# Kernel tuning notes

Measured on AMD Instinct MI355X. Metric: run time of the kernel, lower is better.

Reference implementation:

```python
import jax, jax.numpy as jnp
import numpy as np

N = 100000      # nodes
E = 1600000     # edges (avg degree 16)
FEAT, HID, OUT = 128, 64, 40
P_DROP = 0.5


def setup_inputs() -> dict:
    key = jax.random.key(0)
    ks = jax.random.split(key, 7)
    x = jax.random.normal(ks[0], (N, FEAT), dtype=jnp.float32)
    edge_index = jax.random.randint(ks[1], (2, E), 0, N, dtype=jnp.int32)
    W1 = jax.random.normal(ks[2], (FEAT, HID), dtype=jnp.float32) / np.float32(np.sqrt(FEAT))
    b1 = jnp.zeros((HID,), jnp.float32)
    W2 = jax.random.normal(ks[3], (HID, OUT), dtype=jnp.float32) / np.float32(np.sqrt(HID))
    b2 = jnp.zeros((OUT,), jnp.float32)
    # scaled inverted-dropout mask: values in {0, 1/(1-p)}
    keep = jax.random.bernoulli(ks[4], 1.0 - P_DROP, (N, HID))
    drop_mask = keep.astype(jnp.float32) / np.float32(1.0 - P_DROP)
    return {"x": x, "edge_index": edge_index, "W1": W1, "b1": b1,
            "W2": W2, "b2": b2, "drop_mask": drop_mask}


def _gcn_conv(x, W, b, src, dst):
    """PyG GCNConv: h = xW; add self-loops; sym-normalized scatter-add; +b."""
    h = x @ W                                   # [N, D_out]
    ones = jnp.ones((src.shape[0],), h.dtype)
    deg = jax.ops.segment_sum(ones, dst, num_segments=N) + 1.0  # +1 self-loop
    dinv = jax.lax.rsqrt(deg)                   # deg > 0 due to self-loops
    norm = dinv[src] * dinv[dst]                # [E]
    msg = h[src] * norm[:, None]                # gather + scale
    agg = jax.ops.segment_sum(msg, dst, num_segments=N)
    agg = agg + h * (dinv * dinv)[:, None]      # self-loop contribution
    return agg + b


def reference(x, edge_index, W1, b1, W2, b2, drop_mask):
    src, dst = edge_index[0], edge_index[1]
    h = _gcn_conv(x, W1, b1, src, dst)
    h = jax.nn.relu(h)
    h = h * drop_mask                           # F.dropout (pre-drawn mask)
    out = _gcn_conv(h, W2, b2, src, dst)
    return out
```

## Files before the change

kernel.cpp:

```cpp
#include <hip/hip_runtime.h>
#include <hip/hip_fp16.h>

#define NN     100000
#define NE     1600000
#define FEAT   128
#define HID    64
#define OUTD   40
#define BSH    8
#define BNODES 256
#define NBKT   ((NN + BNODES - 1) / BNODES)
#define CAP    5120
#define CCHUNK 2048

typedef _Float16 half8 __attribute__((ext_vector_type(8)));
typedef float    f32x4 __attribute__((ext_vector_type(4)));

__global__ __launch_bounds__(256) void k_pairs(const int* __restrict__ src,
                                               const int* __restrict__ dst,
                                               int* __restrict__ bfill,
                                               int* __restrict__ pairs) {
    __shared__ int bcnt[NBKT];
    __shared__ int gb[NBKT];
    int t = threadIdx.x;
    for (int i = t; i < NBKT; i += 256) bcnt[i] = 0;
    __syncthreads();
    int e0 = blockIdx.x * CCHUNK;
    int pk[8], bb[8], off[8];
    #pragma unroll
    for (int i = 0; i < 8; ++i) {
        int e = e0 + i * 256 + t;
        if (e < NE) {
            int d = dst[e];
            pk[i]  = (src[e] << BSH) | (d & (BNODES - 1));
            bb[i]  = d >> BSH;
            off[i] = atomicAdd(&bcnt[bb[i]], 1);
        } else bb[i] = -1;
    }
    __syncthreads();
    for (int i = t; i < NBKT; i += 256) {
        int c = bcnt[i];
        gb[i] = c ? (i * CAP + atomicAdd(&bfill[i], c)) : 0;
    }
    __syncthreads();
    #pragma unroll
    for (int i = 0; i < 8; ++i)
        if (bb[i] >= 0) pairs[gb[bb[i]] + off[i]] = pk[i];
}

__global__ __launch_bounds__(256) void k_degdinv(const int* __restrict__ pairs,
                                                 const int* __restrict__ bfill,
                                                 float* __restrict__ dinv) {
    __shared__ int hist[BNODES];
    int b = blockIdx.x, t = threadIdx.x;
    hist[t] = 0;
    __syncthreads();
    int base = b * CAP, count = bfill[b];
    for (int i = t; i < count; i += 256)
        atomicAdd(&hist[pairs[base + i] & (BNODES - 1)], 1);
    __syncthreads();
    int node = (b << BSH) + t;
    if (node < NN) dinv[node] = rsqrtf((float)hist[t] + 1.0f);
}

__global__ __launch_bounds__(256) void k_csr(const int* __restrict__ pairs,
                                             const int* __restrict__ bfill,
                                             const float* __restrict__ dinv,
                                             int* __restrict__ row_beg,
                                             int* __restrict__ row_end,
                                             int2* __restrict__ csr) {
    __shared__ int   nd[BNODES];
    __shared__ int   sc[BNODES];
    __shared__ int   ro[BNODES + 1];
    __shared__ int   cnt2[BNODES];
    __shared__ float ldin[BNODES];
    int b = blockIdx.x, t = threadIdx.x;
    nd[t] = 0; cnt2[t] = 0;
    __syncthreads();
    int base = b * CAP, count = bfill[b];
    for (int i = t; i < count; i += 256)
        atomicAdd(&nd[pairs[base + i] & (BNODES - 1)], 1);
    __syncthreads();
    int v = nd[t];
    ldin[t] = rsqrtf((float)v + 1.0f);
    sc[t] = v;
    __syncthreads();
    for (int off = 1; off < BNODES; off <<= 1) {
        int u = (t >= off) ? sc[t - off] : 0;
        __syncthreads();
        sc[t] += u;
        __syncthreads();
    }
    ro[t + 1] = sc[t];
    if (t == 0) ro[0] = 0;
    __syncthreads();
    int node = (b << BSH) + t;
    if (node < NN) {
        row_beg[node] = base + ro[t];
        row_end[node] = base + sc[t];
    }
    for (int i = t; i < count; i += 256) {
        int p  = pairs[base + i];
        int dl = p & (BNODES - 1);
        int s  = p >> BSH;
        int pos = ro[dl] + atomicAdd(&cnt2[dl], 1);
        csr[base + pos] = make_int2(s, __float_as_int(dinv[s] * ldin[dl]));
    }
}

__global__ __launch_bounds__(256) void k_wprep(const float* __restrict__ W1,
                                               const float* __restrict__ W2,
                                               _Float16* __restrict__ w1f,
                                               _Float16* __restrict__ w2f) {
    int t = threadIdx.x;
    for (int it = t; it < 16 * 64; it += 256) {
        int f = it >> 6, l = it & 63;
        int kk = f >> 2, n = f & 3;
        int krow = kk * 32 + (l >> 4) * 8;
        int col  = n * 16 + (l & 15);
        #pragma unroll
        for (int i = 0; i < 8; ++i)
            w1f[it * 8 + i] = (_Float16)W1[(krow + i) * HID + col];
    }
    for (int it = t; it < 6 * 64; it += 256) {
        int f = it >> 6, l = it & 63;
        int kk = f / 3, n = f - kk * 3;
        int krow = kk * 32 + (l >> 4) * 8;
        int col  = n * 16 + (l & 15);
        #pragma unroll
        for (int i = 0; i < 8; ++i)
            w2f[it * 8 + i] = (col < OUTD) ? (_Float16)W2[(krow + i) * OUTD + col]
                                           : (_Float16)0.f;
    }
}

__global__ __launch_bounds__(256) void k_mgemm1(const float* __restrict__ x,
                                                const _Float16* __restrict__ w1f,
                                                __half* __restrict__ h1h) {
    int wid = (blockIdx.x * 256 + threadIdx.x) >> 6;
    int l = threadIdx.x & 63;
    if (wid >= NN / 16) return;
    half8 bf[4][4];
    #pragma unroll
    for (int kk = 0; kk < 4; ++kk)
        #pragma unroll
        for (int n = 0; n < 4; ++n)
            bf[kk][n] = ((const half8*)w1f)[(kk * 4 + n) * 64 + l];
    f32x4 acc[4] = {};
    int arow = wid * 16 + (l & 15);
    const float* xp = x + (size_t)arow * FEAT + (l >> 4) * 8;
    #pragma unroll
    for (int kk = 0; kk < 4; ++kk) {
        float4 u0 = *(const float4*)(xp + kk * 32);
        float4 u1 = *(const float4*)(xp + kk * 32 + 4);
        half8 af;
        af[0] = (_Float16)u0.x; af[1] = (_Float16)u0.y;
        af[2] = (_Float16)u0.z; af[3] = (_Float16)u0.w;
        af[4] = (_Float16)u1.x; af[5] = (_Float16)u1.y;
        af[6] = (_Float16)u1.z; af[7] = (_Float16)u1.w;
        #pragma unroll
        for (int n = 0; n < 4; ++n)
            acc[n] = __builtin_amdgcn_mfma_f32_16x16x32_f16(af, bf[kk][n], acc[n], 0, 0, 0);
    }
    int orow = wid * 16 + (l >> 4) * 4;
    int ocol = l & 15;
    #pragma unroll
    for (int n = 0; n < 4; ++n)
        #pragma unroll
        for (int r = 0; r < 4; ++r)
            h1h[(size_t)(orow + r) * HID + n * 16 + ocol] = __float2half(acc[n][r]);
}

__global__ __launch_bounds__(256) void k_agg1(const int* __restrict__ row_beg,
                                              const int* __restrict__ row_end,
                                              const int2* __restrict__ csr,
                                              const float* __restrict__ dinv,
                                              const __half* __restrict__ h1h,
                                              const float* __restrict__ b1,
                                              const float* __restrict__ mask,
                                              _Float16* __restrict__ hh) {
    int node = blockIdx.x * 4 + (threadIdx.x >> 6);
    if (node >= NN) return;
    int l = threadIdx.x & 63;
    int beg = __builtin_amdgcn_readfirstlane(row_beg[node]);
    int end = __builtin_amdgcn_readfirstlane(row_end[node]);
    float acc = 0.f;
    int j = beg;
    for (; j + 8 <= end; j += 8) {
        int2 e0 = csr[j+0], e1 = csr[j+1], e2 = csr[j+2], e3 = csr[j+3];
        int2 e4 = csr[j+4], e5 = csr[j+5], e6 = csr[j+6], e7 = csr[j+7];
        float a0 = __half2float(h1h[(size_t)e0.x * HID + l]);
        float a1 = __half2float(h1h[(size_t)e1.x * HID + l]);
        float a2 = __half2float(h1h[(size_t)e2.x * HID + l]);
        float a3 = __half2float(h1h[(size_t)e3.x * HID + l]);
        float a4 = __half2float(h1h[(size_t)e4.x * HID + l]);
        float a5 = __half2float(h1h[(size_t)e5.x * HID + l]);
        float a6 = __half2float(h1h[(size_t)e6.x * HID + l]);
        float a7 = __half2float(h1h[(size_t)e7.x * HID + l]);
        acc = fmaf(a0, __int_as_float(e0.y), acc);
        acc = fmaf(a1, __int_as_float(e1.y), acc);
        acc = fmaf(a2, __int_as_float(e2.y), acc);
        acc = fmaf(a3, __int_as_float(e3.y), acc);
        acc = fmaf(a4, __int_as_float(e4.y), acc);
        acc = fmaf(a5, __int_as_float(e5.y), acc);
        acc = fmaf(a6, __int_as_float(e6.y), acc);
        acc = fmaf(a7, __int_as_float(e7.y), acc);
    }
    for (; j < end; ++j) {
        int2 e = csr[j];
        acc = fmaf(__half2float(h1h[(size_t)e.x * HID + l]), __int_as_float(e.y), acc);
    }
    float di = dinv[node];
    float vv = acc + __half2float(h1h[(size_t)node * HID + l]) * di * di + b1[l];
    vv = vv > 0.f ? vv : 0.f;
    hh[(size_t)node * HID + l] = (_Float16)(vv * mask[(size_t)node * HID + l]);
}

__global__ __launch_bounds__(256) void k_mgemm2(const _Float16* __restrict__ hh,
                                                const _Float16* __restrict__ w2f,
                                                __half* __restrict__ h2h) {
    int wid = (blockIdx.x * 256 + threadIdx.x) >> 6;
    int l = threadIdx.x & 63;
    if (wid >= NN / 16) return;
    half8 bf[2][3];
    #pragma unroll
    for (int kk = 0; kk < 2; ++kk)
        #pragma unroll
        for (int n = 0; n < 3; ++n)
            bf[kk][n] = ((const half8*)w2f)[(kk * 3 + n) * 64 + l];
    f32x4 acc[3] = {};
    int arow = wid * 16 + (l & 15);
    const _Float16* hp = hh + (size_t)arow * HID + (l >> 4) * 8;
    #pragma unroll
    for (int kk = 0; kk < 2; ++kk) {
        half8 af = *(const half8*)(hp + kk * 32);
        #pragma unroll
        for (int n = 0; n < 3; ++n)
            acc[n] = __builtin_amdgcn_mfma_f32_16x16x32_f16(af, bf[kk][n], acc[n], 0, 0, 0);
    }
    int orow = wid * 16 + (l >> 4) * 4;
    int ocol = l & 15;
    #pragma unroll
    for (int n = 0; n < 3; ++n) {
        int col = n * 16 + ocol;
        if (col < OUTD) {
            #pragma unroll
            for (int r = 0; r < 4; ++r)
                h2h[(size_t)(orow + r) * OUTD + col] = __float2half(acc[n][r]);
        }
    }
}

__global__ __launch_bounds__(256) void k_agg2(const int* __restrict__ row_beg,
                                              const int* __restrict__ row_end,
                                              const int2* __restrict__ csr,
                                              const float* __restrict__ dinv,
                                              const __half* __restrict__ h2h,
                                              const float* __restrict__ b2,
                                              float* __restrict__ out) {
    int node = blockIdx.x * 4 + (threadIdx.x >> 6);
    if (node >= NN) return;
    int l = threadIdx.x & 63;
    if (l >= OUTD) return;
    int beg = __builtin_amdgcn_readfirstlane(row_beg[node]);
    int end = __builtin_amdgcn_readfirstlane(row_end[node]);
    float acc = 0.f;
    int j = beg;
    for (; j + 8 <= end; j += 8) {
        int2 e0 = csr[j+0], e1 = csr[j+1], e2 = csr[j+2], e3 = csr[j+3];
        int2 e4 = csr[j+4], e5 = csr[j+5], e6 = csr[j+6], e7 = csr[j+7];
        float a0 = __half2float(h2h[(size_t)e0.x * OUTD + l]);
        float a1 = __half2float(h2h[(size_t)e1.x * OUTD + l]);
        float a2 = __half2float(h2h[(size_t)e2.x * OUTD + l]);
        float a3 = __half2float(h2h[(size_t)e3.x * OUTD + l]);
        float a4 = __half2float(h2h[(size_t)e4.x * OUTD + l]);
        float a5 = __half2float(h2h[(size_t)e5.x * OUTD + l]);
        float a6 = __half2float(h2h[(size_t)e6.x * OUTD + l]);
        float a7 = __half2float(h2h[(size_t)e7.x * OUTD + l]);
        acc = fmaf(a0, __int_as_float(e0.y), acc);
        acc = fmaf(a1, __int_as_float(e1.y), acc);
        acc = fmaf(a2, __int_as_float(e2.y), acc);
        acc = fmaf(a3, __int_as_float(e3.y), acc);
        acc = fmaf(a4, __int_as_float(e4.y), acc);
        acc = fmaf(a5, __int_as_float(e5.y), acc);
        acc = fmaf(a6, __int_as_float(e6.y), acc);
        acc = fmaf(a7, __int_as_float(e7.y), acc);
    }
    for (; j < end; ++j) {
        int2 e = csr[j];
        acc = fmaf(__half2float(h2h[(size_t)e.x * OUTD + l]), __int_as_float(e.y), acc);
    }
    float di = dinv[node];
    out[(size_t)node * OUTD + l] = acc + __half2float(h2h[(size_t)node * OUTD + l]) * di * di + b2[l];
}

extern "C" void kernel_launch(void* const* d_in, const int* in_sizes, int n_in,
                              void* d_out, int out_size, void* d_ws, size_t ws_size,
                              hipStream_t stream) {
    const float* x    = (const float*)d_in[0];
    const int*   ei   = (const int*)d_in[1];
    const int*   src  = ei;
    const int*   dst  = ei + NE;
    const float* W1   = (const float*)d_in[2];
    const float* b1   = (const float*)d_in[3];
    const float* W2   = (const float*)d_in[4];
    const float* b2   = (const float*)d_in[5];
    const float* mask = (const float*)d_in[6];
    float* out = (float*)d_out;

    char* ws = (char*)d_ws;
    int*      bfill   = (int*)ws;          ws += (size_t)NBKT * 4;
    int*      row_beg = (int*)ws;          ws += (size_t)NN * 4;
    int*      row_end = (int*)ws;          ws += (size_t)NN * 4;
    float*    dinv    = (float*)ws;        ws += (size_t)NN * 4;
    _Float16* w1f     = (_Float16*)ws;     ws += 16 * 64 * 8 * 2;
    _Float16* w2f     = (_Float16*)ws;     ws += 6 * 64 * 8 * 2;
    int2*     csr     = (int2*)ws;         ws += (size_t)NBKT * CAP * 8;
    __half*   h1h     = (__half*)ws;       ws += (size_t)NN * HID * 2;
    _Float16* hh      = (_Float16*)ws;     ws += (size_t)NN * HID * 2;
    int*      pairs   = (int*)hh;
    __half*   h2h     = h1h;

    hipMemsetAsync(bfill, 0, (size_t)NBKT * 4, stream);

    k_pairs  <<<(NE + CCHUNK - 1) / CCHUNK, 256, 0, stream>>>(src, dst, bfill, pairs);
    k_degdinv<<<NBKT, 256, 0, stream>>>(pairs, bfill, dinv);
    k_csr    <<<NBKT, 256, 0, stream>>>(pairs, bfill, dinv, row_beg, row_end, csr);
    k_wprep  <<<1, 256, 0, stream>>>(W1, W2, w1f, w2f);

    k_mgemm1 <<<(NN / 16 + 3) / 4, 256, 0, stream>>>(x, w1f, h1h);
    k_agg1   <<<(NN + 3) / 4, 256, 0, stream>>>(row_beg, row_end, csr, dinv,
                                                h1h, b1, mask, hh);
    k_mgemm2 <<<(NN / 16 + 3) / 4, 256, 0, stream>>>(hh, w2f, h2h);
    k_agg2   <<<(NN + 3) / 4, 256, 0, stream>>>(row_beg, row_end, csr, dinv,
                                                h2h, b2, out);
}
```

Before: 204.9 us.

## Aggregate before second GEMM, sort CSR by source, pack dropout mask to bits

Reorders layer 2 so aggregation runs on the 64-wide hidden features before multiplying by W2, which lets bias addition fuse into the GEMM epilogue and removes the separate agg2 kernel. CSR rows are sub-sorted by coarse source-index bucket to improve gather locality in the aggregation kernels. The dropout mask is packed into 64-bit ballots in a separate kernel that still reads the full mask, and the kept-value scale is hardcoded as 2.0, which depends on p=0.5. Layer-2 aggregation now gathers 64 features per edge instead of 40, adding gather traffic.

```diff
diff --git a/kernel.cpp b/kernel.cpp
--- a/kernel.cpp
+++ b/kernel.cpp
@@ -11,6 +11,7 @@
 #define NBKT   ((NN + BNODES - 1) / BNODES)
 #define CAP    5120
 #define CCHUNK 2048
+#define KSUB   8
 
 typedef _Float16 half8 __attribute__((ext_vector_type(8)));
 typedef float    f32x4 __attribute__((ext_vector_type(4)));
@@ -68,43 +69,60 @@
                                              int* __restrict__ row_beg,
                                              int* __restrict__ row_end,
                                              int2* __restrict__ csr) {
-    __shared__ int   nd[BNODES];
-    __shared__ int   sc[BNODES];
-    __shared__ int   ro[BNODES + 1];
-    __shared__ int   cnt2[BNODES];
+    __shared__ int   nd[BNODES * KSUB];
+    __shared__ int   exs[BNODES * KSUB];
+    __shared__ int   part[256];
     __shared__ float ldin[BNODES];
     int b = blockIdx.x, t = threadIdx.x;
-    nd[t] = 0; cnt2[t] = 0;
+    for (int i = t; i < BNODES * KSUB; i += 256) nd[i] = 0;
     __syncthreads();
     int base = b * CAP, count = bfill[b];
-    for (int i = t; i < count; i += 256)
-        atomicAdd(&nd[pairs[base + i] & (BNODES - 1)], 1);
-    __syncthreads();
-    int v = nd[t];
-    ldin[t] = rsqrtf((float)v + 1.0f);
-    sc[t] = v;
-    __syncthreads();
-    for (int off = 1; off < BNODES; off <<= 1) {
-        int u = (t >= off) ? sc[t - off] : 0;
+    for (int i = t; i < count; i += 256) {
+        int p = pairs[base + i];
+        atomicAdd(&nd[(p & (BNODES - 1)) * KSUB + ((p >> BSH) >> 14)], 1);
+    }
+    __syncthreads();
+    int loc[KSUB]; int s0 = 0;
+    #pragma unroll
+    for (int k = 0; k < KSUB; ++k) { loc[k] = s0; s0 += nd[t * KSUB + k]; }
+    part[t] = s0;
+    __syncthreads();
+    for (int off = 1; off < 256; off <<= 1) {
+        int u = (t >= off) ? part[t - off] : 0;
         __syncthreads();
-        sc[t] += u;
+        part[t] += u;
         __syncthreads();
     }
-    ro[t + 1] = sc[t];
-    if (t == 0) ro[0] = 0;
+    int pexcl = part[t] - s0;
+    #pragma unroll
+    for (int k = 0; k < KSUB; ++k) exs[t * KSUB + k] = pexcl + loc[k];
+    ldin[t] = rsqrtf((float)s0 + 1.0f);
     __syncthreads();
     int node = (b << BSH) + t;
     if (node < NN) {
-        row_beg[node] = base + ro[t];
-        row_end[node] = base + sc[t];
-    }
+        row_beg[node] = base + pexcl;
+        row_end[node] = base + pexcl + s0;
+    }
+    for (int i = t; i < BNODES * KSUB; i += 256) nd[i] = 0;
+    __syncthreads();
     for (int i = t; i < count; i += 256) {
         int p  = pairs[base + i];
         int dl = p & (BNODES - 1);
         int s  = p >> BSH;
-        int pos = ro[dl] + atomicAdd(&cnt2[dl], 1);
+        int key = dl * KSUB + (s >> 14);
+        int pos = exs[key] + atomicAdd(&nd[key], 1);
         csr[base + pos] = make_int2(s, __float_as_int(dinv[s] * ldin[dl]));
     }
+}
+
+__global__ __launch_bounds__(256) void k_maskbits(const float* __restrict__ mask,
+                                                  unsigned long long* __restrict__ mb) {
+    int node = blockIdx.x * 4 + (threadIdx.x >> 6);
+    if (node >= NN) return;
+    int l = threadIdx.x & 63;
+    float m = mask[(size_t)node * HID + l];
+    unsigned long long bits = __ballot(m != 0.f);
+    if (l == 0) mb[node] = bits;
 }
 
 __global__ __launch_bounds__(256) void k_wprep(const float* __restrict__ W1,
@@ -170,14 +188,15 @@
             h1h[(size_t)(orow + r) * HID + n * 16 + ocol] = __float2half(acc[n][r]);
 }
 
-__global__ __launch_bounds__(256) void k_agg1(const int* __restrict__ row_beg,
-                                              const int* __restrict__ row_end,
-                                              const int2* __restrict__ csr,
-                                              const float* __restrict__ dinv,
-                                              const __half* __restrict__ h1h,
-                                              const float* __restrict__ b1,
-                                              const float* __restrict__ mask,
-                                              _Float16* __restrict__ hh) {
+template<int MODE>
+__global__ __launch_bounds__(256) void k_agg(const int* __restrict__ row_beg,
+                                             const int* __restrict__ row_end,
+                                             const int2* __restrict__ csr,
+                                             const float* __restrict__ dinv,
+                                             const __half* __restrict__ feat,
+                                             const float* __restrict__ b1,
+                                             const unsigned long long* __restrict__ maskbits,
+                                             _Float16* __restrict__ outp) {
     int node = blockIdx.x * 4 + (threadIdx.x >> 6);
     if (node >= NN) return;
     int l = threadIdx.x & 63;
@@ -188,14 +207,14 @@
     for (; j + 8 <= end; j += 8) {
         int2 e0 = csr[j+0], e1 = csr[j+1], e2 = csr[j+2], e3 = csr[j+3];
         int2 e4 = csr[j+4], e5 = csr[j+5], e6 = csr[j+6], e7 = csr[j+7];
-        float a0 = __half2float(h1h[(size_t)e0.x * HID + l]);
-        float a1 = __half2float(h1h[(size_t)e1.x * HID + l]);
-        float a2 = __half2float(h1h[(size_t)e2.x * HID + l]);
-        float a3 = __half2float(h1h[(size_t)e3.x * HID + l]);
-        float a4 = __half2float(h1h[(size_t)e4.x * HID + l]);
-        float a5 = __half2float(h1h[(size_t)e5.x * HID + l]);
-        float a6 = __half2float(h1h[(size_t)e6.x * HID + l]);
-        float a7 = __half2float(h1h[(size_t)e7.x * HID + l]);
+        float a0 = __half2float(feat[(size_t)e0.x * HID + l]);
+        float a1 = __half2float(feat[(size_t)e1.x * HID + l]);
+        float a2 = __half2float(feat[(size_t)e2.x * HID + l]);
+        float a3 = __half2float(feat[(size_t)e3.x * HID + l]);
+        float a4 = __half2float(feat[(size_t)e4.x * HID + l]);
+        float a5 = __half2float(feat[(size_t)e5.x * HID + l]);
+        float a6 = __half2float(feat[(size_t)e6.x * HID + l]);
+        float a7 = __half2float(feat[(size_t)e7.x * HID + l]);
         acc = fmaf(a0, __int_as_float(e0.y), acc);
         acc = fmaf(a1, __int_as_float(e1.y), acc);
         acc = fmaf(a2, __int_as_float(e2.y), acc);
@@ -207,17 +226,23 @@
     }
     for (; j < end; ++j) {
         int2 e = csr[j];
-        acc = fmaf(__half2float(h1h[(size_t)e.x * HID + l]), __int_as_float(e.y), acc);
+        acc = fmaf(__half2float(feat[(size_t)e.x * HID + l]), __int_as_float(e.y), acc);
     }
     float di = dinv[node];
-    float vv = acc + __half2float(h1h[(size_t)node * HID + l]) * di * di + b1[l];
-    vv = vv > 0.f ? vv : 0.f;
-    hh[(size_t)node * HID + l] = (_Float16)(vv * mask[(size_t)node * HID + l]);
-}
-
-__global__ __launch_bounds__(256) void k_mgemm2(const _Float16* __restrict__ hh,
+    float vv = acc + __half2float(feat[(size_t)node * HID + l]) * di * di;
+    if (MODE == 0) {
+        vv += b1[l];
+        vv = vv > 0.f ? vv : 0.f;
+        unsigned long long mb = maskbits[node];
+        vv *= ((mb >> l) & 1ull) ? 2.0f : 0.0f;
+    }
+    outp[(size_t)node * HID + l] = (_Float16)vv;
+}
+
+__global__ __launch_bounds__(256) void k_mgemm2(const _Float16* __restrict__ aggh,
                                                 const _Float16* __restrict__ w2f,
-                                                __half* __restrict__ h2h) {
+                                                const float* __restrict__ b2,
+                                                float* __restrict__ out) {
     int wid = (blockIdx.x * 256 + threadIdx.x) >> 6;
     int l = threadIdx.x & 63;
     if (wid >= NN / 16) return;
@@ -229,7 +254,7 @@
             bf[kk][n] = ((const half8*)w2f)[(kk * 3 + n) * 64 + l];
     f32x4 acc[3] = {};
     int arow = wid * 16 + (l & 15);
-    const _Float16* hp = hh + (size_t)arow * HID + (l >> 4) * 8;
+    const _Float16* hp = aggh + (size_t)arow * HID + (l >> 4) * 8;
     #pragma unroll
     for (int kk = 0; kk < 2; ++kk) {
         half8 af = *(const half8*)(hp + kk * 32);
@@ -243,54 +268,12 @@
     for (int n = 0; n < 3; ++n) {
         int col = n * 16 + ocol;
         if (col < OUTD) {
+            float bb = b2[col];
             #pragma unroll
             for (int r = 0; r < 4; ++r)
-                h2h[(size_t)(orow + r) * OUTD + col] = __float2half(acc[n][r]);
+                out[(size_t)(orow + r) * OUTD + col] = acc[n][r] + bb;
         }
     }
-}
-
-__global__ __launch_bounds__(256) void k_agg2(const int* __restrict__ row_beg,
-                                              const int* __restrict__ row_end,
-                                              const int2* __restrict__ csr,
-                                              const float* __restrict__ dinv,
-                                              const __half* __restrict__ h2h,
-                                              const float* __restrict__ b2,
-                                              float* __restrict__ out) {
-    int node = blockIdx.x * 4 + (threadIdx.x >> 6);
-    if (node >= NN) return;
-    int l = threadIdx.x & 63;
-    if (l >= OUTD) return;
-    int beg = __builtin_amdgcn_readfirstlane(row_beg[node]);
-    int end = __builtin_amdgcn_readfirstlane(row_end[node]);
-    float acc = 0.f;
-    int j = beg;
-    for (; j + 8 <= end; j += 8) {
-        int2 e0 = csr[j+0], e1 = csr[j+1], e2 = csr[j+2], e3 = csr[j+3];
-        int2 e4 = csr[j+4], e5 = csr[j+5], e6 = csr[j+6], e7 = csr[j+7];
-        float a0 = __half2float(h2h[(size_t)e0.x * OUTD + l]);
-        float a1 = __half2float(h2h[(size_t)e1.x * OUTD + l]);
-        float a2 = __half2float(h2h[(size_t)e2.x * OUTD + l]);
-        float a3 = __half2float(h2h[(size_t)e3.x * OUTD + l]);
-        float a4 = __half2float(h2h[(size_t)e4.x * OUTD + l]);
-        float a5 = __half2float(h2h[(size_t)e5.x * OUTD + l]);
-        float a6 = __half2float(h2h[(size_t)e6.x * OUTD + l]);
-        float a7 = __half2float(h2h[(size_t)e7.x * OUTD + l]);
-        acc = fmaf(a0, __int_as_float(e0.y), acc);
-        acc = fmaf(a1, __int_as_float(e1.y), acc);
-        acc = fmaf(a2, __int_as_float(e2.y), acc);
-        acc = fmaf(a3, __int_as_float(e3.y), acc);
-        acc = fmaf(a4, __int_as_float(e4.y), acc);
-        acc = fmaf(a5, __int_as_float(e5.y), acc);
-        acc = fmaf(a6, __int_as_float(e6.y), acc);
-        acc = fmaf(a7, __int_as_float(e7.y), acc);
-    }
-    for (; j < end; ++j) {
-        int2 e = csr[j];
-        acc = fmaf(__half2float(h2h[(size_t)e.x * OUTD + l]), __int_as_float(e.y), acc);
-    }
-    float di = dinv[node];
-    out[(size_t)node * OUTD + l] = acc + __half2float(h2h[(size_t)node * OUTD + l]) * di * di + b2[l];
 }
 
 extern "C" void kernel_launch(void* const* d_in, const int* in_sizes, int n_in,
@@ -312,25 +295,27 @@
     int*      row_beg = (int*)ws;          ws += (size_t)NN * 4;
     int*      row_end = (int*)ws;          ws += (size_t)NN * 4;
     float*    dinv    = (float*)ws;        ws += (size_t)NN * 4;
+    unsigned long long* maskb = (unsigned long long*)ws; ws += (size_t)NN * 8;
     _Float16* w1f     = (_Float16*)ws;     ws += 16 * 64 * 8 * 2;
     _Float16* w2f     = (_Float16*)ws;     ws += 6 * 64 * 8 * 2;
     int2*     csr     = (int2*)ws;         ws += (size_t)NBKT * CAP * 8;
     __half*   h1h     = (__half*)ws;       ws += (size_t)NN * HID * 2;
     _Float16* hh      = (_Float16*)ws;     ws += (size_t)NN * HID * 2;
     int*      pairs   = (int*)hh;
-    __half*   h2h     = h1h;
+    _Float16* aggh    = (_Float16*)h1h;
 
     hipMemsetAsync(bfill, 0, (size_t)NBKT * 4, stream);
 
-    k_pairs  <<<(NE + CCHUNK - 1) / CCHUNK, 256, 0, stream>>>(src, dst, bfill, pairs);
-    k_degdinv<<<NBKT, 256, 0, stream>>>(pairs, bfill, dinv);
-    k_csr    <<<NBKT, 256, 0, stream>>>(pairs, bfill, dinv, row_beg, row_end, csr);
-    k_wprep  <<<1, 256, 0, stream>>>(W1, W2, w1f, w2f);
-
-    k_mgemm1 <<<(NN / 16 + 3) / 4, 256, 0, stream>>>(x, w1f, h1h);
-    k_agg1   <<<(NN + 3) / 4, 256, 0, stream>>>(row_beg, row_end, csr, dinv,
-                                                h1h, b1, mask, hh);
-    k_mgemm2 <<<(NN / 16 + 3) / 4, 256, 0, stream>>>(hh, w2f, h2h);
-    k_agg2   <<<(NN + 3) / 4, 256, 0, stream>>>(row_beg, row_end, csr, dinv,
-                                                h2h, b2, out);
-}
+    k_pairs   <<<(NE + CCHUNK - 1) / CCHUNK, 256, 0, stream>>>(src, dst, bfill, pairs);
+    k_degdinv <<<NBKT, 256, 0, stream>>>(pairs, bfill, dinv);
+    k_csr     <<<NBKT, 256, 0, stream>>>(pairs, bfill, dinv, row_beg, row_end, csr);
+    k_maskbits<<<(NN + 3) / 4, 256, 0, stream>>>(mask, maskb);
+    k_wprep   <<<1, 256, 0, stream>>>(W1, W2, w1f, w2f);
+
+    k_mgemm1  <<<(NN / 16 + 3) / 4, 256, 0, stream>>>(x, w1f, h1h);
+    k_agg<0>  <<<(NN + 3) / 4, 256, 0, stream>>>(row_beg, row_end, csr, dinv,
+                                                 (const __half*)h1h, b1, maskb, hh);
+    k_agg<1>  <<<(NN + 3) / 4, 256, 0, stream>>>(row_beg, row_end, csr, dinv,
+                                                 (const __half*)hh, nullptr, nullptr, aggh);
+    k_mgemm2  <<<(NN / 16 + 3) / 4, 256, 0, stream>>>(aggh, w2f, b2, out);
+}
```

Result: slower. 218.5 us (+6.6%).
